# Kernel optimization log

Measured on AMD Instinct MI355X. Metric: run time of the kernel, lower is better.

The kernel has to match this reference:

```python
import jax, jax.numpy as jnp
import numpy as np
from jax import lax

B, N, NUM_Q, H = 16, 64, 256, 64


def setup_inputs() -> dict:
    key = jax.random.key(0)
    ks = jax.random.split(key, 12)
    s = 0.05
    return {
        "q": jax.random.randint(ks[0], (B, N), 0, NUM_Q),
        "r": jax.random.randint(ks[1], (B, N), 0, 2),
        "x_emb": jax.random.normal(ks[2], (2 * NUM_Q, H), jnp.float32) * s,
        "q_emb": jax.random.normal(ks[3], (NUM_Q, H), jnp.float32) * s,
        "init_h": jax.random.normal(ks[4], (NUM_Q, H), jnp.float32) * s,
        "w1": jax.random.normal(ks[5], (2 * H, H), jnp.float32) * s,
        "b1": jnp.zeros((H,), jnp.float32),
        "w2": jax.random.normal(ks[6], (H, H), jnp.float32) * s,
        "b2": jnp.zeros((H,), jnp.float32),
        "w_ih": jax.random.normal(ks[7], (3 * H, 2 * H), jnp.float32) * s,
        "w_hh": jax.random.normal(ks[8], (3 * H, H), jnp.float32) * s,
        "b_ih": jnp.zeros((3 * H,), jnp.float32),
        "b_hh": jnp.zeros((3 * H,), jnp.float32),
        "bias": jnp.zeros((1, NUM_Q, 1), jnp.float32),
        "out_w": jax.random.normal(ks[9], (H,), jnp.float32) * s,
        "theta": jnp.asarray(0.0, jnp.float32),
    }


def reference(q, r, x_emb, q_emb, init_h, w1, b1, w2, b2, w_ih, w_hh, b_ih, b_hh, bias, out_w, theta):
    xe = x_emb[q + NUM_Q * r]                          # [B,N,H]
    mask = jax.nn.one_hot(q, NUM_Q, dtype=xe.dtype)    # [B,N,Q] one-hot of answered KC
    ht0 = jnp.broadcast_to(init_h, (B, NUM_Q, H))

    def gru_seq(x):
        # torch nn.GRU(batch_first=True) scanned over the num_q axis, h0 = 0.
        # x: [B,Q,2H] -> [B,Q,H]; gate order (r, z, n).
        gi = jnp.einsum('bqi,gi->bqg', x, w_ih) + b_ih  # [B,Q,3H]

        def cell(h, gi_t):
            gh = h @ w_hh.T + b_hh
            i_r, i_z, i_n = jnp.split(gi_t, 3, axis=-1)
            h_r, h_z, h_n = jnp.split(gh, 3, axis=-1)
            rg = jax.nn.sigmoid(i_r + h_r)
            zg = jax.nn.sigmoid(i_z + h_z)
            ng = jnp.tanh(i_n + rg * h_n)
            hn = (1.0 - zg) * ng + zg * h
            return hn, hn

        _, hs = lax.scan(cell, jnp.zeros((B, H), x.dtype), jnp.swapaxes(gi, 0, 1))
        return jnp.swapaxes(hs, 0, 1)

    def step(ht, inp):
        xe_t, m_t = inp                                  # [B,H], [B,Q]
        m3 = m_t[..., None]
        # aggregate: answered KC gets [h, x_emb], others get [h, q_emb]
        tail = m3 * xe_t[:, None, :] + (1.0 - m3) * q_emb[None]
        ht_cat = jnp.concatenate([ht, tail], axis=-1)    # [B,Q,2H]
        # f_self MLP (dropout = identity in eval); f_neighbor undefined in
        # source (pass) -> shared MLP stand-in, so m = mlp(ht_cat) everywhere.
        m = jnp.maximum(ht_cat @ w1 + b1, 0.0) @ w2 + b2
        ht_new = gru_seq(jnp.concatenate([m, ht], axis=-1))
        return ht_new, ht_new

    _, hs = lax.scan(step, ht0, (jnp.swapaxes(xe, 0, 1), jnp.swapaxes(mask, 0, 1)))
    h_full = jnp.concatenate([ht0[None], hs], axis=0).transpose(1, 0, 2, 3)  # [B,N+1,Q,H]

    # decayed-softmax attention over the growing history, vectorized over t.
    rate = jnp.exp(theta)
    sim = jnp.einsum('btd,cd->btc', q_emb[q], q_emb)     # [B,tau,Q]
    idx = jnp.arange(N)
    dt = idx[:, None] - idx[None, :]                     # t - tau, [N,N]
    decay = jnp.exp(-rate * jnp.maximum(dt, 0).astype(sim.dtype))
    neg = jnp.finfo(sim.dtype).min
    scores = jnp.where((dt >= 0)[None, :, :, None],
                       decay[None, :, :, None] * sim[:, None, :, :], neg)  # [B,t,tau,Q]
    alpha = jax.nn.softmax(scores, axis=2)               # softmax over history tau
    hread = jnp.einsum('btuc,bucf->btcf', alpha, h_full[:, :N])
    h_cur = h_full[:, 1:]                                # state after step t
    logits = jnp.einsum('btcf,f->btc', h_cur + hread, out_w) + bias.reshape(1, 1, NUM_Q)
    y = jax.nn.sigmoid(logits)                           # [B,N,Q]
    return y, h_full
```

## Files before the change

kernel.cpp:

```cpp
#include <hip/hip_runtime.h>
#include <math.h>

#define WS_CB     0
#define WS_QE1    192
#define WS_XE1    16576
#define WS_G      82112
#define WS_HW     147648
#define WS_U16    413888
#define WS_WHH16  422080
#define WS_W2M16  428224
#define WS_I16    434368
#define WS_GFLAG  442560

typedef _Float16 h2 __attribute__((ext_vector_type(2)));

#if defined(__has_builtin)
#if __has_builtin(__builtin_amdgcn_fdot2)
#define FDOT2(a,b,c) __builtin_amdgcn_fdot2((a),(b),(c),false)
#endif
#endif
#ifndef FDOT2
__device__ inline float fdot2_sw(h2 a, h2 b, float c){ return c + (float)a[0]*(float)b[0] + (float)a[1]*(float)b[1]; }
#define FDOT2(a,b,c) fdot2_sw((a),(b),(c))
#endif

__device__ inline h2 H2(unsigned u){ union{unsigned x; h2 h;} v; v.x=u; return v.h; }
__device__ inline unsigned short F2H(float f){ union{_Float16 h; unsigned short s;} v; v.h=(_Float16)f; return v.s; }
__device__ inline unsigned PACK2(float a, float b){ return (unsigned)F2H(a) | ((unsigned)F2H(b)<<16); }

#define SPIN(p,tgt) while (__hip_atomic_load((p), __ATOMIC_ACQUIRE, __HIP_MEMORY_SCOPE_WORKGROUP) < (tgt)) {}
#define WGREL(p,v)  __hip_atomic_store((p), (v), __ATOMIC_RELEASE, __HIP_MEMORY_SCOPE_WORKGROUP)

__global__ __launch_bounds__(256) void kPrep(
    const int* __restrict__ q, const int* __restrict__ r,
    const float* __restrict__ x_emb, const float* __restrict__ q_emb,
    const float* __restrict__ init_h, const float* __restrict__ w1,
    const float* __restrict__ b1, const float* __restrict__ w2,
    const float* __restrict__ b2, const float* __restrict__ w_ih,
    const float* __restrict__ w_hh, const float* __restrict__ b_ih,
    float* __restrict__ ws, float* __restrict__ h_full)
{
  int idx = blockIdx.x*256 + threadIdx.x;
  unsigned* wsu = (unsigned*)ws;
  if (idx < 192) {
    int g = idx; float s = b_ih[g];
    for (int j=0;j<64;j++) s += b2[j]*w_ih[g*128+j];
    ws[WS_CB+g] = s;
  } else if (idx < 16576) {
    int e = idx-192; int c = e>>6, i = e&63;
    float s = b1[i];
    for (int k=0;k<64;k++) s += q_emb[c*64+k]*w1[(64+k)*64+i];
    ws[WS_QE1+e] = s;
  } else if (idx < 82112) {
    int e = idx-16576; int bt = e>>6, i = e&63;
    int row = q[bt] + 256*r[bt];
    float s = b1[i];
    for (int k=0;k<64;k++) s += x_emb[row*64+k]*w1[(64+k)*64+i];
    ws[WS_XE1+e] = s;
  } else if (idx < 147648) {
    int e = idx-82112; int a = e>>8, cc = e&255;
    float s = 0.f;
    for (int d=0;d<64;d++) s += q_emb[a*64+d]*q_emb[cc*64+d];
    ws[WS_G+e] = s;
  } else if (idx < 409792) {
    int e = idx-147648; int bb = e>>14, cf = e&16383;
    h_full[(size_t)bb*65*16384 + cf] = init_h[cf];
  } else if (idx < 417984) {
    int e = idx-409792; int rr = e>>5, d = e&31;
    float v0, v1;
    if (rr < 64) { v0 = w1[(2*d)*64+rr];   v1 = w1[(2*d+1)*64+rr]; }
    else { int g = rr-64; v0 = w_ih[g*128+64+2*d]; v1 = w_ih[g*128+64+2*d+1]; }
    wsu[WS_U16+e] = PACK2(v0,v1);
  } else if (idx < 424128) {
    int e = idx-417984; int g = e>>5, d = e&31;
    wsu[WS_WHH16+e] = PACK2(w_hh[g*64+2*d], w_hh[g*64+2*d+1]);
  } else if (idx < 430272) {
    int e = idx-424128; int g = e>>5, d = e&31;
    float s0=0.f, s1=0.f;
    for (int j=0;j<64;j++){ float wij = w_ih[g*128+j]; s0 += w2[(2*d)*64+j]*wij; s1 += w2[(2*d+1)*64+j]*wij; }
    wsu[WS_W2M16+e] = PACK2(s0,s1);
  }
}

__global__ __launch_bounds__(512,2) void kA(
    const int* __restrict__ q, const float* __restrict__ b_hh,
    float* __restrict__ ws, float* __restrict__ h_full)
{
  __shared__ __align__(16) unsigned short h16s[4][16][64];
  __shared__ __align__(16) unsigned short inbox[16][64];
  __shared__ __align__(16) unsigned short a16s[4][8][64];
  __shared__ float h32s[4][8][64];
  __shared__ __align__(16) float4 gi4s[4][4][64];
  __shared__ int flgH[4], p2s[4];

  const int bid = blockIdx.x, b = bid & 15, tg = bid >> 4;
  const int tid = threadIdx.x, w = tid >> 6, lane = tid & 63;
  const bool isA = (w < 4);
  const int i = isA ? w : (w - 4);
  const int t = tg*4 + i;

  const unsigned* U16  = (const unsigned*)ws + WS_U16;
  const unsigned* WH16 = (const unsigned*)ws + WS_WHH16;
  const unsigned* WM16 = (const unsigned*)ws + WS_W2M16;
  const float* qe1 = ws + WS_QE1;
  const float* xe1 = ws + WS_XE1;
  const float* cb  = ws + WS_CB;
  unsigned* gflag = (unsigned*)ws + WS_GFLAG;
  unsigned* hfu = (unsigned*)h_full;

  if (tid < 4) { flgH[tid] = 0; p2s[tid] = 0; }
  if (isA) h16s[i][15][lane] = 0;
  __syncthreads();

  if (isA) {
    h2 wr[32], wz[32], wn[32], m2r[32], m2z[32];
    #pragma unroll
    for (int d=0; d<32; d++) {
      wr[d]  = H2(WH16[(lane)*32+d]);
      wz[d]  = H2(WH16[(64+lane)*32+d]);
      wn[d]  = H2(WH16[(128+lane)*32+d]);
      m2r[d] = H2(WM16[(lane)*32+d]);
      m2z[d] = H2(WM16[(64+lane)*32+d]);
    }
    const float bhr = b_hh[lane], bhz = b_hh[64+lane], bhn = b_hh[128+lane];
    float hreg = 0.f;

    for (int c=0; c<256; c++) {
      if (((c&3)==0) && i<3) { SPIN(&p2s[i+1], c-12); }
      SPIN(&p2s[i], c+1);
      float4 gv = gi4s[i][c&3][lane];
      float g2r = 0.f, g2z = 0.f;
      {
        const uint4* ap = (const uint4*)a16s[i][c&7];
        #pragma unroll
        for (int k=0;k<8;k++){ uint4 c4 = ap[k];
          h2 p0=H2(c4.x), p1=H2(c4.y), p2=H2(c4.z), p3=H2(c4.w);
          g2r=FDOT2(m2r[4*k+0],p0,g2r); g2r=FDOT2(m2r[4*k+1],p1,g2r); g2r=FDOT2(m2r[4*k+2],p2,g2r); g2r=FDOT2(m2r[4*k+3],p3,g2r);
          g2z=FDOT2(m2z[4*k+0],p0,g2z); g2z=FDOT2(m2z[4*k+1],p1,g2z); g2z=FDOT2(m2z[4*k+2],p2,g2z); g2z=FDOT2(m2z[4*k+3],p3,g2z);
        }
      }
      float ghr = bhr, ghz = bhz, ghn = bhn;
      {
        const uint4* hp = (const uint4*)h16s[i][(c+15)&15];
        #pragma unroll
        for (int k=0;k<8;k++){ uint4 c4 = hp[k];
          h2 p0=H2(c4.x), p1=H2(c4.y), p2=H2(c4.z), p3=H2(c4.w);
          ghr=FDOT2(wr[4*k+0],p0,ghr); ghr=FDOT2(wr[4*k+1],p1,ghr); ghr=FDOT2(wr[4*k+2],p2,ghr); ghr=FDOT2(wr[4*k+3],p3,ghr);
          ghz=FDOT2(wz[4*k+0],p0,ghz); ghz=FDOT2(wz[4*k+1],p1,ghz); ghz=FDOT2(wz[4*k+2],p2,ghz); ghz=FDOT2(wz[4*k+3],p3,ghz);
          ghn=FDOT2(wn[4*k+0],p0,ghn); ghn=FDOT2(wn[4*k+1],p1,ghn); ghn=FDOT2(wn[4*k+2],p2,ghn); ghn=FDOT2(wn[4*k+3],p3,ghn);
        }
      }
      float rg = 1.f/(1.f+__expf(-(gv.x + g2r + ghr)));
      float zg = 1.f/(1.f+__expf(-(gv.y + g2z + ghz)));
      float xn = gv.z + rg*ghn;
      float e2 = __expf(2.f*xn);
      float ng = 1.f - 2.f/(e2+1.f);
      hreg = zg*hreg + (1.f-zg)*ng;
      h16s[i][c&15][lane] = F2H(hreg);
      h32s[i][c&7][lane]  = hreg;
      if (lane == 0) WGREL(&flgH[i], c+1);
    }
  } else {
    h2 u0[32],u1[32],u2[32],u3[32],w2n[32];
    #pragma unroll
    for (int d=0; d<32; d++) {
      u0[d]  = H2(U16[(lane)*32+d]);
      u1[d]  = H2(U16[(64+lane)*32+d]);
      u2[d]  = H2(U16[(128+lane)*32+d]);
      u3[d]  = H2(U16[(192+lane)*32+d]);
      w2n[d] = H2(WM16[(128+lane)*32+d]);
    }
    const float cbr = cb[lane], cbz = cb[64+lane], cbn = cb[128+lane];
    const int qrow = q[b*64+t];
    const float xr = xe1[(b*64+t)*64+lane];
    const unsigned* hfp = hfu + (size_t)(b*65 + 4*tg)*16384;
    float*    hfoF = h_full + (size_t)(b*65 + t + 1)*16384;
    unsigned* hfoU = hfu + (size_t)(b*65 + t + 1)*16384;
    unsigned* gfp = gflag + (b*16 + tg - 1);
    unsigned* gfc = gflag + (b*16 + tg);
    const bool needFlag = (i==3) && (tg < 15);
    unsigned gv = 0;

    if (i == 0) {
      if (tg > 0) {
        while ((gv = __hip_atomic_load(gfp, __ATOMIC_RELAXED, __HIP_MEMORY_SCOPE_AGENT)) < 4u)
          __builtin_amdgcn_s_sleep(1);
      }
      for (int rr=0; rr<4; rr++) {
        union{unsigned u; float f;} cv;
        cv.u = __hip_atomic_load(&hfp[rr*64+lane], __ATOMIC_RELAXED, __HIP_MEMORY_SCOPE_AGENT);
        inbox[rr][lane] = F2H(cv.f);
      }
    }
    float e1cur = (qrow == 0) ? xr : qe1[lane];
    float prP=0.f, pzP=0.f, pnP=0.f;

    for (int s=0; s<=260; s++) {
      int tgt = s-4; if (tgt > 256) tgt = 256;
      SPIN(&flgH[i], tgt);
      float vrow = 0.f;
      const bool havePf = (i==0) && (s+4 <= 255);
      if (havePf) {
        if (tg > 0) {
          while (gv < (unsigned)(s+5)) {
            gv = __hip_atomic_load(gfp, __ATOMIC_RELAXED, __HIP_MEMORY_SCOPE_AGENT);
            if (gv < (unsigned)(s+5)) __builtin_amdgcn_s_sleep(1);
          }
        }
        union{unsigned u; float f;} cv;
        cv.u = __hip_atomic_load(&hfp[(s+4)*64+lane], __ATOMIC_RELAXED, __HIP_MEMORY_SCOPE_AGENT);
        vrow = cv.f;
      }
      float pr=0.f, pz=0.f, pn=0.f;
      if (s <= 255) {
        if (i > 0) { SPIN(&flgH[i-1], s+1); }
        const uint4* rp = (const uint4*)((i==0) ? inbox[s&15] : h16s[i-1][s&15]);
        float m1 = e1cur; pr = cbr; pz = cbz; pn = cbn;
        #pragma unroll
        for (int k=0;k<8;k++){ uint4 c4 = rp[k];
          h2 p0=H2(c4.x), p1=H2(c4.y), p2=H2(c4.z), p3=H2(c4.w);
          m1=FDOT2(u0[4*k+0],p0,m1); m1=FDOT2(u0[4*k+1],p1,m1); m1=FDOT2(u0[4*k+2],p2,m1); m1=FDOT2(u0[4*k+3],p3,m1);
          pr=FDOT2(u1[4*k+0],p0,pr); pr=FDOT2(u1[4*k+1],p1,pr); pr=FDOT2(u1[4*k+2],p2,pr); pr=FDOT2(u1[4*k+3],p3,pr);
          pz=FDOT2(u2[4*k+0],p0,pz); pz=FDOT2(u2[4*k+1],p1,pz); pz=FDOT2(u2[4*k+2],p2,pz); pz=FDOT2(u2[4*k+3],p3,pz);
          pn=FDOT2(u3[4*k+0],p0,pn); pn=FDOT2(u3[4*k+1],p1,pn); pn=FDOT2(u3[4*k+2],p2,pn); pn=FDOT2(u3[4*k+3],p3,pn);
        }
        float av = fmaxf(m1, 0.f);
        a16s[i][s&7][lane] = F2H(av);
      }
      if (s >= 1 && s <= 256) {
        int sm = s-1;
        float g2n = 0.f;
        const uint4* ap = (const uint4*)a16s[i][sm&7];
        #pragma unroll
        for (int k=0;k<8;k++){ uint4 c4 = ap[k];
          g2n=FDOT2(w2n[4*k+0],H2(c4.x),g2n); g2n=FDOT2(w2n[4*k+1],H2(c4.y),g2n);
          g2n=FDOT2(w2n[4*k+2],H2(c4.z),g2n); g2n=FDOT2(w2n[4*k+3],H2(c4.w),g2n);
        }
        gi4s[i][sm&3][lane] = make_float4(prP, pzP, pnP + g2n, 0.f);
      }
      if (s <= 255) { prP = pr; pzP = pz; pnP = pn; }
      int r = s-5;
      if (r >= 0) {
        float hv = h32s[i][r&7][lane];
        if (i == 3) {
          union{float f; unsigned u;} cu; cu.f = hv;
          __hip_atomic_store(&hfoU[r*64+lane], cu.u, __ATOMIC_RELAXED, __HIP_MEMORY_SCOPE_AGENT);
        } else {
          hfoF[r*64+lane] = hv;
        }
        if (needFlag && ((r&3)==3)) {
          asm volatile("s_waitcnt vmcnt(0)" ::: "memory");
          if (lane == 0) __hip_atomic_store(gfc, (unsigned)(r+1), __ATOMIC_RELAXED, __HIP_MEMORY_SCOPE_AGENT);
        }
      }
      if (havePf) inbox[(s+4)&15][lane] = F2H(vrow);
      if (lane == 0) WGREL(&p2s[i], s);
      if (s < 255) e1cur = ((s+1) == qrow) ? xr : qe1[(s+1)*64+lane];
    }
  }
}

__global__ __launch_bounds__(256) void kHw(const float* __restrict__ h_full,
    const float* __restrict__ out_w, float* __restrict__ hw)
{
  __shared__ float ow[64];
  if (threadIdx.x < 64) ow[threadIdx.x] = out_w[threadIdx.x];
  __syncthreads();
  const int blk = blockIdx.x, c = threadIdx.x;
  const float* hp = h_full + ((size_t)blk*256 + c)*64;
  float s = 0.f;
  #pragma unroll
  for (int f=0; f<64; f++) s += hp[f]*ow[f];
  hw[blk*256+c] = s;
}

__global__ __launch_bounds__(256) void kY(const int* __restrict__ q,
    const float* __restrict__ ws, const float* __restrict__ bias,
    const float* __restrict__ theta, float* __restrict__ y)
{
  const float* G  = ws + WS_G;
  const float* hw = ws + WS_HW;
  const int b = blockIdx.x >> 2, tq = blockIdx.x & 3;
  const int c = threadIdx.x;
  __shared__ float siml[64][256];
  for (int u=0; u<64; u++) {
    int qq = q[b*64+u];
    siml[u][c] = G[qq*256+c];
  }
  __syncthreads();
  const float rate = __expf(theta[0]);
  const float bv = bias[c];
  const float* hwb = hw + b*65*256;
  for (int tt=0; tt<16; tt++) {
    const int t = tq*16+tt;
    float mx = -1e30f;
    for (int u=0; u<=t; u++) {
      float s = __expf(-rate*(float)(t-u))*siml[u][c];
      mx = fmaxf(mx, s);
    }
    float se = 0.f, sw = 0.f;
    for (int u=0; u<=t; u++) {
      float s = __expf(-rate*(float)(t-u))*siml[u][c];
      float e = __expf(s-mx);
      se += e; sw += e*hwb[u*256+c];
    }
    float lg = hwb[(t+1)*256+c] + sw/se + bv;
    y[(b*64+t)*256+c] = 1.f/(1.f+__expf(-lg));
  }
}

extern "C" void kernel_launch(void* const* d_in, const int* in_sizes, int n_in,
                              void* d_out, int out_size, void* d_ws, size_t ws_size,
                              hipStream_t stream)
{
  (void)in_sizes; (void)n_in; (void)out_size; (void)ws_size;
  const int*   q      = (const int*)  d_in[0];
  const int*   r      = (const int*)  d_in[1];
  const float* x_emb  = (const float*)d_in[2];
  const float* q_emb  = (const float*)d_in[3];
  const float* init_h = (const float*)d_in[4];
  const float* w1     = (const float*)d_in[5];
  const float* b1     = (const float*)d_in[6];
  const float* w2     = (const float*)d_in[7];
  const float* b2     = (const float*)d_in[8];
  const float* w_ih   = (const float*)d_in[9];
  const float* w_hh   = (const float*)d_in[10];
  const float* b_ih   = (const float*)d_in[11];
  const float* b_hh   = (const float*)d_in[12];
  const float* bias   = (const float*)d_in[13];
  const float* out_w  = (const float*)d_in[14];
  const float* theta  = (const float*)d_in[15];

  float* out    = (float*)d_out;
  float* y      = out;
  float* h_full = out + 262144;
  float* ws     = (float*)d_ws;

  hipMemsetAsync((unsigned*)ws + WS_GFLAG, 0, 256*sizeof(unsigned), stream);
  kPrep<<<1681,256,0,stream>>>(q,r,x_emb,q_emb,init_h,w1,b1,w2,b2,w_ih,w_hh,b_ih,ws,h_full);
  {
    void* ka[] = { (void*)&q, (void*)&b_hh, (void*)&ws, (void*)&h_full };
    hipError_t e = hipLaunchCooperativeKernel((const void*)kA, dim3(256), dim3(512), ka, 0, stream);
    if (e != hipSuccess) {
      kA<<<dim3(256),dim3(512),0,stream>>>(q,b_hh,ws,h_full);
    }
  }
  kHw<<<1040,256,0,stream>>>(h_full, out_w, ws + WS_HW);
  kY<<<64,256,0,stream>>>(q, ws, bias, theta, y);
}
```

Before: 844.3 us.

## Restructure GRU producer/consumer pipeline with decoupled writeback and deeper buffers

Measured after the change: 795.8 us. -5.7%, faster.

```diff
diff --git a/kernel.cpp b/kernel.cpp
--- a/kernel.cpp
+++ b/kernel.cpp
@@ -9,7 +9,6 @@
 #define WS_U16    413888
 #define WS_WHH16  422080
 #define WS_W2M16  428224
-#define WS_I16    434368
 #define WS_GFLAG  442560
 
 typedef _Float16 h2 __attribute__((ext_vector_type(2)));
@@ -28,8 +27,48 @@
 __device__ inline unsigned short F2H(float f){ union{_Float16 h; unsigned short s;} v; v.h=(_Float16)f; return v.s; }
 __device__ inline unsigned PACK2(float a, float b){ return (unsigned)F2H(a) | ((unsigned)F2H(b)<<16); }
 
-#define SPIN(p,tgt) while (__hip_atomic_load((p), __ATOMIC_ACQUIRE, __HIP_MEMORY_SCOPE_WORKGROUP) < (tgt)) {}
-#define WGREL(p,v)  __hip_atomic_store((p), (v), __ATOMIC_RELEASE, __HIP_MEMORY_SCOPE_WORKGROUP)
+#define F32(X,A) X(A,0)X(A,1)X(A,2)X(A,3)X(A,4)X(A,5)X(A,6)X(A,7)X(A,8)X(A,9)X(A,10)X(A,11)X(A,12)X(A,13)X(A,14)X(A,15)X(A,16)X(A,17)X(A,18)X(A,19)X(A,20)X(A,21)X(A,22)X(A,23)X(A,24)X(A,25)X(A,26)X(A,27)X(A,28)X(A,29)X(A,30)X(A,31)
+#define DCL1(W,K) h2 W##_##K;
+#define DECLW(W) F32(DCL1,W)
+#define LD1(W,K) W##_##K = H2(_wb[K]);
+#define LOADW(W,BASE) { const unsigned* _wb=(BASE); F32(LD1,W) }
+#define DT1(W,K) _acc = FDOT2(W##_##K, H2(RC##K), _acc);
+#define DOTW(ACC,W) { float _acc=(ACC); F32(DT1,W) (ACC)=_acc; }
+#define RC0 qq0.x
+#define RC1 qq0.y
+#define RC2 qq0.z
+#define RC3 qq0.w
+#define RC4 qq1.x
+#define RC5 qq1.y
+#define RC6 qq1.z
+#define RC7 qq1.w
+#define RC8 qq2.x
+#define RC9 qq2.y
+#define RC10 qq2.z
+#define RC11 qq2.w
+#define RC12 qq3.x
+#define RC13 qq3.y
+#define RC14 qq3.z
+#define RC15 qq3.w
+#define RC16 qq4.x
+#define RC17 qq4.y
+#define RC18 qq4.z
+#define RC19 qq4.w
+#define RC20 qq5.x
+#define RC21 qq5.y
+#define RC22 qq5.z
+#define RC23 qq5.w
+#define RC24 qq6.x
+#define RC25 qq6.y
+#define RC26 qq6.z
+#define RC27 qq6.w
+#define RC28 qq7.x
+#define RC29 qq7.y
+#define RC30 qq7.z
+#define RC31 qq7.w
+#define LOADROW(P) { const uint4* _rp=(const uint4*)(P); qq0=_rp[0];qq1=_rp[1];qq2=_rp[2];qq3=_rp[3];qq4=_rp[4];qq5=_rp[5];qq6=_rp[6];qq7=_rp[7]; }
+
+#define POLLGE(F,T) do{ while(*(volatile int*)&(F) < (T)) {} asm volatile("" ::: "memory"); }while(0)
 
 __global__ __launch_bounds__(256) void kPrep(
     const int* __restrict__ q, const int* __restrict__ r,
@@ -87,16 +126,16 @@
     float* __restrict__ ws, float* __restrict__ h_full)
 {
   __shared__ __align__(16) unsigned short h16s[4][16][64];
+  __shared__ __align__(16) unsigned short a16s[4][8][64];
   __shared__ __align__(16) unsigned short inbox[16][64];
-  __shared__ __align__(16) unsigned short a16s[4][8][64];
+  __shared__ __align__(16) float4 gi4s[4][8][64];
   __shared__ float h32s[4][8][64];
-  __shared__ __align__(16) float4 gi4s[4][4][64];
-  __shared__ int flgH[4], p2s[4];
-
-  const int bid = blockIdx.x, b = bid & 15, tg = bid >> 4;
-  const int tid = threadIdx.x, w = tid >> 6, lane = tid & 63;
-  const bool isA = (w < 4);
-  const int i = isA ? w : (w - 4);
+  __shared__ int flgH[4], p2s[4], ioPr[4];
+
+  const int bid=blockIdx.x, b=bid&15, tg=bid>>4;
+  const int tid=threadIdx.x, w=tid>>6, lane=tid&63;
+  const bool isA = (w<4);
+  const int i = isA? w : w-4;
   const int t = tg*4 + i;
 
   const unsigned* U16  = (const unsigned*)ws + WS_U16;
@@ -106,156 +145,146 @@
   const float* xe1 = ws + WS_XE1;
   const float* cb  = ws + WS_CB;
   unsigned* gflag = (unsigned*)ws + WS_GFLAG;
-  unsigned* hfu = (unsigned*)h_full;
-
-  if (tid < 4) { flgH[tid] = 0; p2s[tid] = 0; }
-  if (isA) h16s[i][15][lane] = 0;
+
+  if (tid<4){ flgH[tid]=0; p2s[tid]=0; ioPr[tid]=0; }
+  if (isA) h16s[i][15][lane]=0;
   __syncthreads();
 
+  uint4 qq0,qq1,qq2,qq3,qq4,qq5,qq6,qq7;
+
   if (isA) {
-    h2 wr[32], wz[32], wn[32], m2r[32], m2z[32];
-    #pragma unroll
-    for (int d=0; d<32; d++) {
-      wr[d]  = H2(WH16[(lane)*32+d]);
-      wz[d]  = H2(WH16[(64+lane)*32+d]);
-      wn[d]  = H2(WH16[(128+lane)*32+d]);
-      m2r[d] = H2(WM16[(lane)*32+d]);
-      m2z[d] = H2(WM16[(64+lane)*32+d]);
-    }
-    const float bhr = b_hh[lane], bhz = b_hh[64+lane], bhn = b_hh[128+lane];
-    float hreg = 0.f;
-
-    for (int c=0; c<256; c++) {
-      if (((c&3)==0) && i<3) { SPIN(&p2s[i+1], c-12); }
-      SPIN(&p2s[i], c+1);
-      float4 gv = gi4s[i][c&3][lane];
-      float g2r = 0.f, g2z = 0.f;
-      {
-        const uint4* ap = (const uint4*)a16s[i][c&7];
-        #pragma unroll
-        for (int k=0;k<8;k++){ uint4 c4 = ap[k];
-          h2 p0=H2(c4.x), p1=H2(c4.y), p2=H2(c4.z), p3=H2(c4.w);
-          g2r=FDOT2(m2r[4*k+0],p0,g2r); g2r=FDOT2(m2r[4*k+1],p1,g2r); g2r=FDOT2(m2r[4*k+2],p2,g2r); g2r=FDOT2(m2r[4*k+3],p3,g2r);
-          g2z=FDOT2(m2z[4*k+0],p0,g2z); g2z=FDOT2(m2z[4*k+1],p1,g2z); g2z=FDOT2(m2z[4*k+2],p2,g2z); g2z=FDOT2(m2z[4*k+3],p3,g2z);
+    DECLW(wrq) DECLW(wzq) DECLW(wnq) DECLW(mrq) DECLW(mzq)
+    LOADW(wrq, WH16+lane*32)
+    LOADW(wzq, WH16+(64+lane)*32)
+    LOADW(wnq, WH16+(128+lane)*32)
+    LOADW(mrq, WM16+lane*32)
+    LOADW(mzq, WM16+(64+lane)*32)
+    const float bhr=b_hh[lane], bhz=b_hh[64+lane], bhn=b_hh[128+lane];
+    float hreg=0.f;
+    for (int c=0;c<256;c++){
+      if (((c&7)==0) && i<3) POLLGE(p2s[i+1], c-8);
+      if ((c&3)==0) POLLGE(ioPr[i], c-4);
+      LOADROW(h16s[i][(c+15)&15])
+      float ghr=bhr, ghz=bhz, ghn=bhn;
+      DOTW(ghr,wrq) DOTW(ghz,wzq) DOTW(ghn,wnq)
+      POLLGE(p2s[i], c+1);
+      float4 gv = gi4s[i][c&7][lane];
+      LOADROW(a16s[i][c&7])
+      float g2r=0.f, g2z=0.f;
+      DOTW(g2r,mrq) DOTW(g2z,mzq)
+      float rg = 1.f/(1.f+__expf(-(gv.x+g2r+ghr)));
+      float zg = 1.f/(1.f+__expf(-(gv.y+g2z+ghz)));
+      float xn = gv.z + rg*ghn;
+      float e2 = __expf(2.f*xn);
+      float ng = 1.f-2.f/(e2+1.f);
+      hreg = zg*hreg + (1.f-zg)*ng;
+      h16s[i][c&15][lane]=F2H(hreg);
+      h32s[i][c&7][lane]=hreg;
+      asm volatile("s_waitcnt lgkmcnt(0)" ::: "memory");
+      if (lane==0) *(volatile int*)&flgH[i]=c+1;
+    }
+  } else {
+    DECLW(u0q) DECLW(u1q) DECLW(u2q) DECLW(u3q) DECLW(w2q)
+    LOADW(u0q, U16+lane*32)
+    LOADW(u1q, U16+(64+lane)*32)
+    LOADW(u2q, U16+(128+lane)*32)
+    LOADW(u3q, U16+(192+lane)*32)
+    LOADW(w2q, WM16+(128+lane)*32)
+    const float cbr=cb[lane], cbz=cb[64+lane], cbn=cb[128+lane];
+    const int qrow=q[b*64+t];
+    const float xr=xe1[(b*64+t)*64+lane];
+    const float* hfp = h_full + (size_t)(b*65+4*tg)*16384;
+    float* hfoF = h_full + (size_t)(b*65+t+1)*16384;
+    unsigned* hfoU = (unsigned*)hfoF;
+    unsigned* gfp = gflag + (b*16+tg-1);
+    unsigned* gfc = gflag + (b*16+tg);
+    const bool pubG = (i==3) && (tg<15);
+    unsigned gv=0; int pfrow=0, cp=0;
+    float e1cur = (qrow==0)? xr : qe1[lane];
+    float prP=0.f,pzP=0.f,pnP=0.f;
+
+    for (int s=0;s<=256;s++){
+      if ((s&3)==0) POLLGE(flgH[i], s-4);
+      float e1n=0.f;
+      if (s<255) e1n = ((s+1)==qrow)? xr : qe1[(s+1)*64+lane];
+      float pr=0.f,pz=0.f,pn=0.f;
+      if (s<=255){
+        if (i==0){
+          while (pfrow<=s){
+            if (tg>0){
+              while (gv < (unsigned)(pfrow+1)){
+                gv = __hip_atomic_load(gfp,__ATOMIC_RELAXED,__HIP_MEMORY_SCOPE_AGENT);
+                if (gv < (unsigned)(pfrow+1)) __builtin_amdgcn_s_sleep(1);
+              }
+              union{unsigned u; float f;} cv;
+              cv.u = __hip_atomic_load((const unsigned*)&hfp[pfrow*64+lane],__ATOMIC_RELAXED,__HIP_MEMORY_SCOPE_AGENT);
+              inbox[pfrow&15][lane]=F2H(cv.f);
+            } else {
+              inbox[pfrow&15][lane]=F2H(hfp[pfrow*64+lane]);
+            }
+            pfrow++;
+          }
+          if (pfrow<=s+8){
+            bool can=(tg==0);
+            if (tg>0){
+              if (gv>=(unsigned)(pfrow+1)) can=true;
+              else if ((s&1)==0){ gv=__hip_atomic_load(gfp,__ATOMIC_RELAXED,__HIP_MEMORY_SCOPE_AGENT); can = gv>=(unsigned)(pfrow+1); }
+            }
+            if (can){
+              if (tg>0){
+                union{unsigned u; float f;} cv;
+                cv.u = __hip_atomic_load((const unsigned*)&hfp[pfrow*64+lane],__ATOMIC_RELAXED,__HIP_MEMORY_SCOPE_AGENT);
+                inbox[pfrow&15][lane]=F2H(cv.f);
+              } else {
+                inbox[pfrow&15][lane]=F2H(hfp[pfrow*64+lane]);
+              }
+              pfrow++;
+            }
+          }
+        } else {
+          POLLGE(flgH[i-1], s+1);
+        }
+        LOADROW( (i==0)? inbox[s&15] : h16s[i-1][s&15] )
+        float m1=e1cur; pr=cbr; pz=cbz; pn=cbn;
+        DOTW(m1,u0q) DOTW(pr,u1q) DOTW(pz,u2q) DOTW(pn,u3q)
+        a16s[i][s&7][lane]=F2H(fmaxf(m1,0.f));
+      }
+      if (s>=1){
+        LOADROW(a16s[i][(s-1)&7])
+        float g2n=0.f; DOTW(g2n,w2q)
+        gi4s[i][(s-1)&7][lane]=make_float4(prP,pzP,pnP+g2n,0.f);
+      }
+      asm volatile("s_waitcnt lgkmcnt(0)" ::: "memory");
+      if (lane==0) *(volatile int*)&p2s[i]=s;
+      prP=pr; pzP=pz; pnP=pn; e1cur=e1n;
+      int av=*(volatile int*)&flgH[i];
+      asm volatile("" ::: "memory");
+      int nc=0;
+      while (cp<av && nc<2){
+        float hv=h32s[i][cp&7][lane];
+        if (i==3){ union{float f; unsigned u;} cu; cu.f=hv;
+          __hip_atomic_store(&hfoU[cp*64+lane],cu.u,__ATOMIC_RELAXED,__HIP_MEMORY_SCOPE_AGENT);
+        } else hfoF[cp*64+lane]=hv;
+        cp++; nc++;
+        if ((cp&3)==0){
+          *(volatile int*)&ioPr[i]=cp;
+          if (pubG){ asm volatile("s_waitcnt vmcnt(0)" ::: "memory");
+            if (lane==0) __hip_atomic_store(gfc,(unsigned)cp,__ATOMIC_RELAXED,__HIP_MEMORY_SCOPE_AGENT); }
         }
       }
-      float ghr = bhr, ghz = bhz, ghn = bhn;
-      {
-        const uint4* hp = (const uint4*)h16s[i][(c+15)&15];
-        #pragma unroll
-        for (int k=0;k<8;k++){ uint4 c4 = hp[k];
-          h2 p0=H2(c4.x), p1=H2(c4.y), p2=H2(c4.z), p3=H2(c4.w);
-          ghr=FDOT2(wr[4*k+0],p0,ghr); ghr=FDOT2(wr[4*k+1],p1,ghr); ghr=FDOT2(wr[4*k+2],p2,ghr); ghr=FDOT2(wr[4*k+3],p3,ghr);
-          ghz=FDOT2(wz[4*k+0],p0,ghz); ghz=FDOT2(wz[4*k+1],p1,ghz); ghz=FDOT2(wz[4*k+2],p2,ghz); ghz=FDOT2(wz[4*k+3],p3,ghz);
-          ghn=FDOT2(wn[4*k+0],p0,ghn); ghn=FDOT2(wn[4*k+1],p1,ghn); ghn=FDOT2(wn[4*k+2],p2,ghn); ghn=FDOT2(wn[4*k+3],p3,ghn);
-        }
+    }
+    while (cp<256){
+      POLLGE(flgH[i], cp+1);
+      float hv=h32s[i][cp&7][lane];
+      if (i==3){ union{float f; unsigned u;} cu; cu.f=hv;
+        __hip_atomic_store(&hfoU[cp*64+lane],cu.u,__ATOMIC_RELAXED,__HIP_MEMORY_SCOPE_AGENT);
+      } else hfoF[cp*64+lane]=hv;
+      cp++;
+      if ((cp&3)==0){
+        *(volatile int*)&ioPr[i]=cp;
+        if (pubG){ asm volatile("s_waitcnt vmcnt(0)" ::: "memory");
+          if (lane==0) __hip_atomic_store(gfc,(unsigned)cp,__ATOMIC_RELAXED,__HIP_MEMORY_SCOPE_AGENT); }
       }
-      float rg = 1.f/(1.f+__expf(-(gv.x + g2r + ghr)));
-      float zg = 1.f/(1.f+__expf(-(gv.y + g2z + ghz)));
-      float xn = gv.z + rg*ghn;
-      float e2 = __expf(2.f*xn);
-      float ng = 1.f - 2.f/(e2+1.f);
-      hreg = zg*hreg + (1.f-zg)*ng;
-      h16s[i][c&15][lane] = F2H(hreg);
-      h32s[i][c&7][lane]  = hreg;
-      if (lane == 0) WGREL(&flgH[i], c+1);
-    }
-  } else {
-    h2 u0[32],u1[32],u2[32],u3[32],w2n[32];
-    #pragma unroll
-    for (int d=0; d<32; d++) {
-      u0[d]  = H2(U16[(lane)*32+d]);
-      u1[d]  = H2(U16[(64+lane)*32+d]);
-      u2[d]  = H2(U16[(128+lane)*32+d]);
-      u3[d]  = H2(U16[(192+lane)*32+d]);
-      w2n[d] = H2(WM16[(128+lane)*32+d]);
-    }
-    const float cbr = cb[lane], cbz = cb[64+lane], cbn = cb[128+lane];
-    const int qrow = q[b*64+t];
-    const float xr = xe1[(b*64+t)*64+lane];
-    const unsigned* hfp = hfu + (size_t)(b*65 + 4*tg)*16384;
-    float*    hfoF = h_full + (size_t)(b*65 + t + 1)*16384;
-    unsigned* hfoU = hfu + (size_t)(b*65 + t + 1)*16384;
-    unsigned* gfp = gflag + (b*16 + tg - 1);
-    unsigned* gfc = gflag + (b*16 + tg);
-    const bool needFlag = (i==3) && (tg < 15);
-    unsigned gv = 0;
-
-    if (i == 0) {
-      if (tg > 0) {
-        while ((gv = __hip_atomic_load(gfp, __ATOMIC_RELAXED, __HIP_MEMORY_SCOPE_AGENT)) < 4u)
-          __builtin_amdgcn_s_sleep(1);
-      }
-      for (int rr=0; rr<4; rr++) {
-        union{unsigned u; float f;} cv;
-        cv.u = __hip_atomic_load(&hfp[rr*64+lane], __ATOMIC_RELAXED, __HIP_MEMORY_SCOPE_AGENT);
-        inbox[rr][lane] = F2H(cv.f);
-      }
-    }
-    float e1cur = (qrow == 0) ? xr : qe1[lane];
-    float prP=0.f, pzP=0.f, pnP=0.f;
-
-    for (int s=0; s<=260; s++) {
-      int tgt = s-4; if (tgt > 256) tgt = 256;
-      SPIN(&flgH[i], tgt);
-      float vrow = 0.f;
-      const bool havePf = (i==0) && (s+4 <= 255);
-      if (havePf) {
-        if (tg > 0) {
-          while (gv < (unsigned)(s+5)) {
-            gv = __hip_atomic_load(gfp, __ATOMIC_RELAXED, __HIP_MEMORY_SCOPE_AGENT);
-            if (gv < (unsigned)(s+5)) __builtin_amdgcn_s_sleep(1);
-          }
-        }
-        union{unsigned u; float f;} cv;
-        cv.u = __hip_atomic_load(&hfp[(s+4)*64+lane], __ATOMIC_RELAXED, __HIP_MEMORY_SCOPE_AGENT);
-        vrow = cv.f;
-      }
-      float pr=0.f, pz=0.f, pn=0.f;
-      if (s <= 255) {
-        if (i > 0) { SPIN(&flgH[i-1], s+1); }
-        const uint4* rp = (const uint4*)((i==0) ? inbox[s&15] : h16s[i-1][s&15]);
-        float m1 = e1cur; pr = cbr; pz = cbz; pn = cbn;
-        #pragma unroll
-        for (int k=0;k<8;k++){ uint4 c4 = rp[k];
-          h2 p0=H2(c4.x), p1=H2(c4.y), p2=H2(c4.z), p3=H2(c4.w);
-          m1=FDOT2(u0[4*k+0],p0,m1); m1=FDOT2(u0[4*k+1],p1,m1); m1=FDOT2(u0[4*k+2],p2,m1); m1=FDOT2(u0[4*k+3],p3,m1);
-          pr=FDOT2(u1[4*k+0],p0,pr); pr=FDOT2(u1[4*k+1],p1,pr); pr=FDOT2(u1[4*k+2],p2,pr); pr=FDOT2(u1[4*k+3],p3,pr);
-          pz=FDOT2(u2[4*k+0],p0,pz); pz=FDOT2(u2[4*k+1],p1,pz); pz=FDOT2(u2[4*k+2],p2,pz); pz=FDOT2(u2[4*k+3],p3,pz);
-          pn=FDOT2(u3[4*k+0],p0,pn); pn=FDOT2(u3[4*k+1],p1,pn); pn=FDOT2(u3[4*k+2],p2,pn); pn=FDOT2(u3[4*k+3],p3,pn);
-        }
-        float av = fmaxf(m1, 0.f);
-        a16s[i][s&7][lane] = F2H(av);
-      }
-      if (s >= 1 && s <= 256) {
-        int sm = s-1;
-        float g2n = 0.f;
-        const uint4* ap = (const uint4*)a16s[i][sm&7];
-        #pragma unroll
-        for (int k=0;k<8;k++){ uint4 c4 = ap[k];
-          g2n=FDOT2(w2n[4*k+0],H2(c4.x),g2n); g2n=FDOT2(w2n[4*k+1],H2(c4.y),g2n);
-          g2n=FDOT2(w2n[4*k+2],H2(c4.z),g2n); g2n=FDOT2(w2n[4*k+3],H2(c4.w),g2n);
-        }
-        gi4s[i][sm&3][lane] = make_float4(prP, pzP, pnP + g2n, 0.f);
-      }
-      if (s <= 255) { prP = pr; pzP = pz; pnP = pn; }
-      int r = s-5;
-      if (r >= 0) {
-        float hv = h32s[i][r&7][lane];
-        if (i == 3) {
-          union{float f; unsigned u;} cu; cu.f = hv;
-          __hip_atomic_store(&hfoU[r*64+lane], cu.u, __ATOMIC_RELAXED, __HIP_MEMORY_SCOPE_AGENT);
-        } else {
-          hfoF[r*64+lane] = hv;
-        }
-        if (needFlag && ((r&3)==3)) {
-          asm volatile("s_waitcnt vmcnt(0)" ::: "memory");
-          if (lane == 0) __hip_atomic_store(gfc, (unsigned)(r+1), __ATOMIC_RELAXED, __HIP_MEMORY_SCOPE_AGENT);
-        }
-      }
-      if (havePf) inbox[(s+4)&15][lane] = F2H(vrow);
-      if (lane == 0) WGREL(&p2s[i], s);
-      if (s < 255) e1cur = ((s+1) == qrow) ? xr : qe1[(s+1)*64+lane];
     }
   }
 }
```
